# Kernel tuning notes

Measured on AMD Instinct MI355X. Metric: run time of the kernel, lower is better.

Reference implementation:

```python
import jax, jax.numpy as jnp
import numpy as np

N, E, F, D, L, C = 100000, 1600000, 64, 64, 3, 10
BN_EPS = 1e-5


def _batchnorm(h, gamma, beta):
    # training-mode BatchNorm1d: biased batch stats over the node dim
    mu = jnp.mean(h, axis=0)
    var = jnp.mean(jnp.square(h - mu), axis=0)
    return (h - mu) * jax.lax.rsqrt(var + BN_EPS) * gamma + beta


def setup_inputs() -> dict:
    key = jax.random.key(0)
    ks = jax.random.split(key, 6)
    x = jax.random.normal(ks[0], (N, F), jnp.float32)
    edge_index = jax.random.randint(ks[1], (2, E), 0, N, dtype=jnp.int64)
    W1 = jax.random.normal(ks[2], (L, F, D), jnp.float32) * 0.1
    W2 = jax.random.normal(ks[3], (L, D, D), jnp.float32) * 0.1
    fcW = jax.random.normal(ks[4], (L + 1, D, C), jnp.float32) * 0.1
    return {
        "x": x,
        "edge_index": edge_index,
        "W1": W1,
        "b1": jnp.zeros((L, D), jnp.float32),
        "g1": jnp.ones((L, D), jnp.float32),
        "be1": jnp.zeros((L, D), jnp.float32),
        "W2": W2,
        "b2": jnp.zeros((L, D), jnp.float32),
        "gbn": jnp.ones((L, D), jnp.float32),
        "bbn": jnp.zeros((L, D), jnp.float32),
        "fcW": fcW,
        "fcb": jnp.zeros((L + 1, C), jnp.float32),
    }


def reference(x, edge_index, W1, b1, g1, be1, W2, b2, gbn, bbn, fcW, fcb):
    src, dst = edge_index[0], edge_index[1]
    outs = [x]
    h = x
    for i in range(L):
        # GINConv (eps=0): mlp(h + sum_{j in N(i)} h_j)
        agg = jax.ops.segment_sum(h[src], dst, num_segments=N)
        z = (h + agg) @ W1[i] + b1[i]
        z = jax.nn.relu(_batchnorm(z, g1[i], be1[i]))
        z = z @ W2[i] + b2[i]
        # outer BN + ReLU
        h = jax.nn.relu(_batchnorm(z, gbn[i], bbn[i]))
        outs.append(h)
    # jumping-knowledge sum of per-layer classifier heads
    logits = outs[0] @ fcW[0] + fcb[0]
    for i in range(1, L + 1):
        logits = logits + outs[i] @ fcW[i] + fcb[i]
    return jax.nn.log_softmax(logits, axis=-1)
```

## Files before the change

### kernel.cpp

```cpp
#include <hip/hip_runtime.h>
#include <math.h>


#define BN_EPS 1e-5f
#define NBKT 256
#define BCAP 12288
#define PCHUNK 4096

typedef __attribute__((ext_vector_type(8))) short bf16x8;
typedef __attribute__((ext_vector_type(4))) float f32x4;

__device__ __forceinline__ float bf2f(unsigned short u) {
  return __uint_as_float(((unsigned int)u) << 16);
}
__device__ __forceinline__ unsigned short f2bf(float x) {
  unsigned int b = __float_as_uint(x);
  return (unsigned short)((b + 0x7FFFu + ((b >> 16) & 1u)) >> 16);
}

__device__ __forceinline__ float stat8(const float* __restrict__ st, int i) {
  float s = 0.f;
#pragma unroll
  for (int k = 0; k < 8; k++) s += st[k * 128 + i];
  return s;
}


__global__ __launch_bounds__(256) void k_prep(
    const float* __restrict__ W1, const float* __restrict__ W2,
    const float* __restrict__ fcW, unsigned short* __restrict__ wh,
    unsigned short* __restrict__ wl, unsigned short* __restrict__ bh,
    unsigned short* __restrict__ bl) {
  int g = blockIdx.x * 256 + threadIdx.x;
  if (g < 6 * 4096) {
    int m = g >> 12, rem = g & 4095;
    int k = rem >> 6, n = rem & 63;
    const float* W = (m & 1) ? (W2 + (m >> 1) * 4096) : (W1 + (m >> 1) * 4096);
    float w = W[k * 64 + n];
    unsigned short hi = f2bf(w);
    float resid = w - bf2f(hi);
    int kx = (((k >> 3) ^ (n & 7)) << 3) + (k & 7);
    wh[m * 4096 + n * 64 + kx] = hi;
    wl[m * 4096 + n * 64 + kx] = f2bf(resid);
  } else {
    int g2 = g - 6 * 4096;
    if (g2 < 4 * 1024) {
      int l = g2 >> 10, rem = g2 & 1023;
      int n = rem & 15, k = rem >> 4;
      float w = (n < 10) ? fcW[l * 640 + k * 10 + n] : 0.f;
      unsigned short hi = f2bf(w);
      float resid = w - bf2f(hi);
      int idx = l * 1024 + n * 64 + (((k >> 3) ^ (n & 7)) << 3) + (k & 7);
      bh[idx] = hi;
      bl[idx] = f2bf(resid);
    }
  }
}


__global__ __launch_bounds__(256) void k_part_conv(
    const int* __restrict__ src, const int* __restrict__ dst,
    int* __restrict__ bcur, int2* __restrict__ ep, int E, int nparts,
    const float* __restrict__ x, unsigned short* __restrict__ x16, int N) {
  __shared__ int lh[NBKT];
  __shared__ int lbase[NBKT];
  __shared__ int lcur[NBKT];
  int tid = threadIdx.x;
  if ((int)blockIdx.x < nparts) {
    int base = blockIdx.x * PCHUNK;
    int end = min(base + PCHUNK, E);
    lh[tid] = 0;
    lcur[tid] = 0;
    __syncthreads();
    for (int e = base + tid; e < end; e += 256) atomicAdd(&lh[dst[e] >> 9], 1);
    __syncthreads();
    int c = lh[tid];
    lbase[tid] = c ? (tid * BCAP + atomicAdd(&bcur[tid], c)) : 0;
    __syncthreads();
    for (int e = base + tid; e < end; e += 256) {
      int d = dst[e];
      int b = d >> 9;
      int r = atomicAdd(&lcur[b], 1);
      ep[lbase[b] + r] = make_int2(src[e], d);
    }
  } else {
    size_t g = ((size_t)blockIdx.x - nparts) * 256 + tid;
    size_t base = g * 8;
    if (base + 8 <= (size_t)N * 64) {
      float4 t0 = *(const float4*)(x + base);
      float4 t1 = *(const float4*)(x + base + 4);
      *(ushort4*)(x16 + base) =
          make_ushort4(f2bf(t0.x), f2bf(t0.y), f2bf(t0.z), f2bf(t0.w));
      *(ushort4*)(x16 + base + 4) =
          make_ushort4(f2bf(t1.x), f2bf(t1.y), f2bf(t1.z), f2bf(t1.w));
    }
  }
}

__global__ __launch_bounds__(256) void k_bucketsort(
    const int2* __restrict__ ep, const int* __restrict__ bcur,
    int* __restrict__ offs, int* __restrict__ bend, int* __restrict__ csr,
    float* __restrict__ stats) {
  __shared__ int cnt[512];
  __shared__ int ts[256];
  __shared__ int cur[512];
  int t = threadIdx.x;
  int b = blockIdx.x;
  if (b == 0) {
    for (int i = t; i < 6144; i += 256) stats[i] = 0.f;
  }
  int lo = b * BCAP;
  int hi = lo + bcur[b];
  cnt[t] = 0;
  cnt[t + 256] = 0;
  __syncthreads();
  for (int e = lo + t; e < hi; e += 256) atomicAdd(&cnt[ep[e].y & 511], 1);
  __syncthreads();
  int c0 = cnt[2 * t], c1 = cnt[2 * t + 1];
  int s = c0 + c1;
  ts[t] = s;
  __syncthreads();
  for (int o = 1; o < 256; o <<= 1) {
    int add = (t >= o) ? ts[t - o] : 0;
    __syncthreads();
    ts[t] += add;
    __syncthreads();
  }
  int excl = ts[t] - s;
  cur[2 * t] = excl;
  cur[2 * t + 1] = excl + c0;
  int n0 = b << 9;
  offs[n0 + 2 * t] = lo + excl;
  offs[n0 + 2 * t + 1] = lo + excl + c0;
  if (t == 255) bend[b] = lo + ts[255];
  __syncthreads();
  for (int e = lo + t; e < hi; e += 256) {
    int2 p = ep[e];
    int pos = atomicAdd(&cur[p.y & 511], 1);
    csr[lo + pos] = p.x;
  }
}


__device__ __forceinline__ float gather_plain(
    const unsigned short* __restrict__ h16, const int* __restrict__ csr,
    int e0, int e1, int lane) {
  float acc = 0.f;
  int e = e0;
  for (; e + 16 <= e1; e += 16) {
    int s0 = csr[e], s1 = csr[e + 1], s2 = csr[e + 2], s3 = csr[e + 3];
    int s4 = csr[e + 4], s5 = csr[e + 5], s6 = csr[e + 6], s7 = csr[e + 7];
    int s8 = csr[e + 8], s9 = csr[e + 9], sa = csr[e + 10], sb = csr[e + 11];
    int sc = csr[e + 12], sd = csr[e + 13], se = csr[e + 14], sf = csr[e + 15];
    float a0 = bf2f(h16[(size_t)s0 * 64 + lane]);
    float a1 = bf2f(h16[(size_t)s1 * 64 + lane]);
    float a2 = bf2f(h16[(size_t)s2 * 64 + lane]);
    float a3 = bf2f(h16[(size_t)s3 * 64 + lane]);
    float a4 = bf2f(h16[(size_t)s4 * 64 + lane]);
    float a5 = bf2f(h16[(size_t)s5 * 64 + lane]);
    float a6 = bf2f(h16[(size_t)s6 * 64 + lane]);
    float a7 = bf2f(h16[(size_t)s7 * 64 + lane]);
    float a8 = bf2f(h16[(size_t)s8 * 64 + lane]);
    float a9 = bf2f(h16[(size_t)s9 * 64 + lane]);
    float aa = bf2f(h16[(size_t)sa * 64 + lane]);
    float ab = bf2f(h16[(size_t)sb * 64 + lane]);
    float ac = bf2f(h16[(size_t)sc * 64 + lane]);
    float ad = bf2f(h16[(size_t)sd * 64 + lane]);
    float ae = bf2f(h16[(size_t)se * 64 + lane]);
    float af = bf2f(h16[(size_t)sf * 64 + lane]);
    acc += (((a0 + a1) + (a2 + a3)) + ((a4 + a5) + (a6 + a7))) +
           (((a8 + a9) + (aa + ab)) + ((ac + ad) + (ae + af)));
  }
  for (; e + 4 <= e1; e += 4) {
    int s0 = csr[e], s1 = csr[e + 1], s2 = csr[e + 2], s3 = csr[e + 3];
    float a0 = bf2f(h16[(size_t)s0 * 64 + lane]);
    float a1 = bf2f(h16[(size_t)s1 * 64 + lane]);
    float a2 = bf2f(h16[(size_t)s2 * 64 + lane]);
    float a3 = bf2f(h16[(size_t)s3 * 64 + lane]);
    acc += (a0 + a1) + (a2 + a3);
  }
  for (; e < e1; e++) acc += bf2f(h16[(size_t)csr[e] * 64 + lane]);
  return acc;
}

__global__ __launch_bounds__(256) void k_agg(
    const unsigned short* __restrict__ h16, const int* __restrict__ offs,
    const int* __restrict__ bend, const int* __restrict__ csr,
    unsigned short* __restrict__ vout, int N) {
  int gid = blockIdx.x * blockDim.x + threadIdx.x;
  int wid = __builtin_amdgcn_readfirstlane(gid >> 6);
  int lane = threadIdx.x & 63;
  if (wid >= N) return;
  int e0 = offs[wid];
  int e1 = ((wid & 511) == 511) ? bend[wid >> 9] : offs[wid + 1];
  float acc = bf2f(h16[(size_t)wid * 64 + lane]) +
              gather_plain(h16, csr, e0, e1, lane);
  vout[(size_t)wid * 64 + lane] = f2bf(acc);
}

__global__ __launch_bounds__(256) void k_aggbn(
    const unsigned short* __restrict__ z16,
    const float* __restrict__ stats_in, const float* __restrict__ gv,
    const float* __restrict__ bev,
    const int* __restrict__ offs, const int* __restrict__ bend,
    const int* __restrict__ csr, unsigned short* __restrict__ vout, int N) {
  __shared__ float ABs[128];
  int tid = threadIdx.x;
  if (tid < 64) {
    float inv_n = 1.f / (float)N;
    float mu = stat8(stats_in, tid) * inv_n;
    float var = stat8(stats_in, 64 + tid) * inv_n - mu * mu;
    float A = rsqrtf(var + BN_EPS) * gv[tid];
    ABs[tid] = A;
    ABs[64 + tid] = bev[tid] - mu * A;
  }
  __syncthreads();
  int gid = blockIdx.x * blockDim.x + tid;
  int wid = __builtin_amdgcn_readfirstlane(gid >> 6);
  int lane = tid & 63;
  if (wid >= N) return;
  float A = ABs[lane], B = ABs[64 + lane];
  float acc = fmaxf(bf2f(z16[(size_t)wid * 64 + lane]) * A + B, 0.f);
  int e0 = offs[wid];
  int e1 = ((wid & 511) == 511) ? bend[wid >> 9] : offs[wid + 1];
  int e = e0;
  for (; e + 16 <= e1; e += 16) {
    int s0 = csr[e], s1 = csr[e + 1], s2 = csr[e + 2], s3 = csr[e + 3];
    int s4 = csr[e + 4], s5 = csr[e + 5], s6 = csr[e + 6], s7 = csr[e + 7];
    int s8 = csr[e + 8], s9 = csr[e + 9], sa = csr[e + 10], sb = csr[e + 11];
    int sc = csr[e + 12], sd = csr[e + 13], se = csr[e + 14], sf = csr[e + 15];
    float a0 = bf2f(z16[(size_t)s0 * 64 + lane]);
    float a1 = bf2f(z16[(size_t)s1 * 64 + lane]);
    float a2 = bf2f(z16[(size_t)s2 * 64 + lane]);
    float a3 = bf2f(z16[(size_t)s3 * 64 + lane]);
    float a4 = bf2f(z16[(size_t)s4 * 64 + lane]);
    float a5 = bf2f(z16[(size_t)s5 * 64 + lane]);
    float a6 = bf2f(z16[(size_t)s6 * 64 + lane]);
    float a7 = bf2f(z16[(size_t)s7 * 64 + lane]);
    float a8 = bf2f(z16[(size_t)s8 * 64 + lane]);
    float a9 = bf2f(z16[(size_t)s9 * 64 + lane]);
    float aa = bf2f(z16[(size_t)sa * 64 + lane]);
    float ab = bf2f(z16[(size_t)sb * 64 + lane]);
    float ac = bf2f(z16[(size_t)sc * 64 + lane]);
    float ad = bf2f(z16[(size_t)sd * 64 + lane]);
    float ae = bf2f(z16[(size_t)se * 64 + lane]);
    float af = bf2f(z16[(size_t)sf * 64 + lane]);
    a0 = fmaxf(a0 * A + B, 0.f); a1 = fmaxf(a1 * A + B, 0.f);
    a2 = fmaxf(a2 * A + B, 0.f); a3 = fmaxf(a3 * A + B, 0.f);
    a4 = fmaxf(a4 * A + B, 0.f); a5 = fmaxf(a5 * A + B, 0.f);
    a6 = fmaxf(a6 * A + B, 0.f); a7 = fmaxf(a7 * A + B, 0.f);
    a8 = fmaxf(a8 * A + B, 0.f); a9 = fmaxf(a9 * A + B, 0.f);
    aa = fmaxf(aa * A + B, 0.f); ab = fmaxf(ab * A + B, 0.f);
    ac = fmaxf(ac * A + B, 0.f); ad = fmaxf(ad * A + B, 0.f);
    ae = fmaxf(ae * A + B, 0.f); af = fmaxf(af * A + B, 0.f);
    acc += (((a0 + a1) + (a2 + a3)) + ((a4 + a5) + (a6 + a7))) +
           (((a8 + a9) + (aa + ab)) + ((ac + ad) + (ae + af)));
  }
  for (; e + 4 <= e1; e += 4) {
    int s0 = csr[e], s1 = csr[e + 1], s2 = csr[e + 2], s3 = csr[e + 3];
    float a0 = bf2f(z16[(size_t)s0 * 64 + lane]);
    float a1 = bf2f(z16[(size_t)s1 * 64 + lane]);
    float a2 = bf2f(z16[(size_t)s2 * 64 + lane]);
    float a3 = bf2f(z16[(size_t)s3 * 64 + lane]);
    a0 = fmaxf(a0 * A + B, 0.f); a1 = fmaxf(a1 * A + B, 0.f);
    a2 = fmaxf(a2 * A + B, 0.f); a3 = fmaxf(a3 * A + B, 0.f);
    acc += (a0 + a1) + (a2 + a3);
  }
  for (; e < e1; e++) {
    float a = bf2f(z16[(size_t)csr[e] * 64 + lane]);
    acc += fmaxf(a * A + B, 0.f);
  }
  vout[(size_t)wid * 64 + lane] = f2bf(acc);
}

__global__ __launch_bounds__(256) void k_gemm2(
    const unsigned short* __restrict__ vin, unsigned short* __restrict__ zout,
    const unsigned short* __restrict__ Wh, const unsigned short* __restrict__ Wl,
    const float* __restrict__ stats_in, const float* __restrict__ gv,
    const float* __restrict__ bev, int dobn,
    float* __restrict__ stats_out, int N) {
  __shared__ float ABs[128];
  __shared__ float red[512];
  int tid = threadIdx.x;
  int n0 = blockIdx.x * 256;
  if (dobn) {
    if (tid < 64) {
      float inv_n = 1.f / (float)N;
      float mu = stat8(stats_in, tid) * inv_n;
      float var = stat8(stats_in, 64 + tid) * inv_n - mu * mu;
      float A = rsqrtf(var + BN_EPS) * gv[tid];
      ABs[tid] = A;
      ABs[64 + tid] = bev[tid] - mu * A;
    }
    __syncthreads();
  }

  int wv = tid >> 6;
  int lane = tid & 63;
  int c = lane & 15;
  int q = lane >> 4;
  int wrow = n0 + wv * 64;

  bf16x8 afrag[4][2];
#pragma unroll
  for (int mt = 0; mt < 4; mt++) {
    int row = wrow + mt * 16 + c;
#pragma unroll
    for (int kb = 0; kb < 2; kb++) {
      int col0 = kb * 32 + q * 8;
      bf16x8 a = {0, 0, 0, 0, 0, 0, 0, 0};
      if (row < N) {
        a = *(const bf16x8*)(vin + (size_t)row * 64 + col0);
        if (dobn) {
#pragma unroll
          for (int j = 0; j < 8; j++) {
            float f = bf2f((unsigned short)a[j]) * ABs[col0 + j] +
                      ABs[64 + col0 + j];
            a[j] = (short)f2bf(fmaxf(f, 0.f));
          }
        }
      }
      afrag[mt][kb] = a;
    }
  }

  f32x4 acc[4][4];
#pragma unroll
  for (int mt = 0; mt < 4; mt++)
#pragma unroll
    for (int nt = 0; nt < 4; nt++)
      acc[mt][nt] = (f32x4){0.f, 0.f, 0.f, 0.f};

#pragma unroll
  for (int nt = 0; nt < 4; nt++) {
    int cn = nt * 16 + c;
#pragma unroll
    for (int kb = 0; kb < 2; kb++) {
      int kchunk = kb * 4 + q;
      int kx = ((kchunk ^ (cn & 7)) << 3);
      bf16x8 bhi = *(const bf16x8*)(Wh + cn * 64 + kx);
      bf16x8 blo = *(const bf16x8*)(Wl + cn * 64 + kx);
#pragma unroll
      for (int mt = 0; mt < 4; mt++) {
        acc[mt][nt] = __builtin_amdgcn_mfma_f32_16x16x32_bf16(
            afrag[mt][kb], bhi, acc[mt][nt], 0, 0, 0);
        acc[mt][nt] = __builtin_amdgcn_mfma_f32_16x16x32_bf16(
            afrag[mt][kb], blo, acc[mt][nt], 0, 0, 0);
      }
    }
  }

#pragma unroll
  for (int mt = 0; mt < 4; mt++) {
#pragma unroll
    for (int r = 0; r < 4; r++) {
      int row = wrow + mt * 16 + q * 4 + r;
      if (row < N) {
        unsigned short* zr = zout + (size_t)row * 64 + c;
        zr[0] = f2bf(acc[mt][0][r]);
        zr[16] = f2bf(acc[mt][1][r]);
        zr[32] = f2bf(acc[mt][2][r]);
        zr[48] = f2bf(acc[mt][3][r]);
      }
    }
  }

  float cs[4], cq[4];
#pragma unroll
  for (int nt = 0; nt < 4; nt++) {
    float s = 0.f, s2 = 0.f;
#pragma unroll
    for (int mt = 0; mt < 4; mt++)
#pragma unroll
      for (int r = 0; r < 4; r++) {
        float v = acc[mt][nt][r];
        s += v;
        s2 += v * v;
      }
    s += __shfl_xor(s, 16);
    s += __shfl_xor(s, 32);
    s2 += __shfl_xor(s2, 16);
    s2 += __shfl_xor(s2, 32);
    cs[nt] = s;
    cq[nt] = s2;
  }
  if (lane < 16) {
#pragma unroll
    for (int nt = 0; nt < 4; nt++) {
      red[wv * 128 + nt * 16 + lane] = cs[nt];
      red[wv * 128 + 64 + nt * 16 + lane] = cq[nt];
    }
  }
  __syncthreads();
  if (tid < 64) {
    float a = red[tid] + red[128 + tid] + red[256 + tid] + red[384 + tid];
    float b = red[64 + tid] + red[192 + tid] + red[320 + tid] + red[448 + tid];
    float* so = stats_out + (blockIdx.x & 7) * 128;
    atomicAdd(&so[tid], a);
    atomicAdd(&so[64 + tid], b);
  }
}

__global__ __launch_bounds__(256) void k_head_mfma(
    const unsigned short* __restrict__ x16,
    const unsigned short* __restrict__ z0, const unsigned short* __restrict__ z1,
    const unsigned short* __restrict__ z2, const float* __restrict__ stats,
    const float* __restrict__ gbn, const float* __restrict__ bbn,
    const unsigned short* __restrict__ bh, const unsigned short* __restrict__ bl,
    const float* __restrict__ fcb, float* __restrict__ out, int N) {
  __shared__ float ABs[3 * 128];
  int tid = threadIdx.x;
  if (tid < 64) {
    float inv_n = 1.f / (float)N;
#pragma unroll
    for (int l = 0; l < 3; l++) {
      const float* st = stats + (2 * l + 1) * 1024;
      float mu = stat8(st, tid) * inv_n;
      float var = stat8(st, 64 + tid) * inv_n - mu * mu;
      float A = rsqrtf(var + BN_EPS) * gbn[l * 64 + tid];
      ABs[l * 128 + tid] = A;
      ABs[l * 128 + 64 + tid] = bbn[l * 64 + tid] - mu * A;
    }
  }
  __syncthreads();

  int wv = tid >> 6, lane = tid & 63;
  int c = lane & 15, q = lane >> 4;
  int wrow = blockIdx.x * 128 + wv * 32;

  f32x4 acc[2];
  acc[0] = (f32x4){0.f, 0.f, 0.f, 0.f};
  acc[1] = (f32x4){0.f, 0.f, 0.f, 0.f};
#pragma unroll
  for (int l = 0; l < 4; l++) {
    const unsigned short* z = (l == 0) ? x16 : (l == 1) ? z0 : (l == 2) ? z1
                                                                       : z2;
#pragma unroll
    for (int kb = 0; kb < 2; kb++) {
      int kchunk = kb * 4 + q;
      int kx = ((kchunk ^ (c & 7)) << 3);
      bf16x8 bh_ = *(const bf16x8*)(bh + l * 1024 + c * 64 + kx);
      bf16x8 bl_ = *(const bf16x8*)(bl + l * 1024 + c * 64 + kx);
      int col0 = kb * 32 + q * 8;
#pragma unroll
      for (int mt = 0; mt < 2; mt++) {
        int row = wrow + mt * 16 + c;
        bf16x8 a = {0, 0, 0, 0, 0, 0, 0, 0};
        if (row < N) {
          a = *(const bf16x8*)(z + (size_t)row * 64 + col0);
          if (l > 0) {
            const float* AB = ABs + (l - 1) * 128;
#pragma unroll
            for (int j = 0; j < 8; j++) {
              float f = bf2f((unsigned short)a[j]) * AB[col0 + j] +
                        AB[64 + col0 + j];
              a[j] = (short)f2bf(fmaxf(f, 0.f));
            }
          }
        }
        acc[mt] = __builtin_amdgcn_mfma_f32_16x16x32_bf16(a, bh_, acc[mt],
                                                          0, 0, 0);
        acc[mt] = __builtin_amdgcn_mfma_f32_16x16x32_bf16(a, bl_, acc[mt],
                                                          0, 0, 0);
      }
    }
  }
  float cb = 0.f;
  if (c < 10) cb = fcb[c] + fcb[10 + c] + fcb[20 + c] + fcb[30 + c];
#pragma unroll
  for (int mt = 0; mt < 2; mt++) {
    float v[4], vm[4];
#pragma unroll
    for (int r = 0; r < 4; r++) {
      v[r] = acc[mt][r] + cb;
      vm[r] = (c < 10) ? v[r] : -INFINITY;
    }
#pragma unroll
    for (int off = 1; off < 16; off <<= 1) {
#pragma unroll
      for (int r = 0; r < 4; r++) vm[r] = fmaxf(vm[r], __shfl_xor(vm[r], off));
    }
    float sm[4];
#pragma unroll
    for (int r = 0; r < 4; r++) sm[r] = (c < 10) ? expf(v[r] - vm[r]) : 0.f;
#pragma unroll
    for (int off = 1; off < 16; off <<= 1) {
#pragma unroll
      for (int r = 0; r < 4; r++) sm[r] += __shfl_xor(sm[r], off);
    }
#pragma unroll
    for (int r = 0; r < 4; r++) {
      int row = wrow + mt * 16 + q * 4 + r;
      if (row < N && c < 10)
        out[(size_t)row * 10 + c] = v[r] - (logf(sm[r]) + vm[r]);
    }
  }
}

extern "C" void kernel_launch(void* const* d_in, const int* in_sizes, int n_in,
                              void* d_out, int out_size, void* d_ws, size_t ws_size,
                              hipStream_t stream) {
  const float* x = (const float*)d_in[0];
  const int* ei = (const int*)d_in[1];
  const float* W1 = (const float*)d_in[2];
  const float* g1 = (const float*)d_in[4];
  const float* be1 = (const float*)d_in[5];
  const float* W2 = (const float*)d_in[6];
  const float* gbn = (const float*)d_in[8];
  const float* bbn = (const float*)d_in[9];
  const float* fcW = (const float*)d_in[10];
  const float* fcb = (const float*)d_in[11];
  float* out = (float*)d_out;

  const int N = in_sizes[0] / 64;
  const int E = in_sizes[1] / 2;
  const int* src = ei;
  const int* dst = ei + E;

  char* ws = (char*)d_ws;
  size_t off = 0;
  auto alloc = [&](size_t bytes) -> void* {
    void* p = ws + off;
    off = (off + bytes + 255) & ~(size_t)255;
    return p;
  };
  int* bcur = (int*)alloc(NBKT * 4);
  float* stats = (float*)alloc(6 * 1024 * 4);
  int* offs = (int*)alloc((size_t)NBKT * 512 * 4);
  int* bend = (int*)alloc(NBKT * 4);
  int* csr = (int*)alloc((size_t)NBKT * BCAP * 4);
  unsigned short* w16h = (unsigned short*)alloc(6 * 4096 * 2);
  unsigned short* w16l = (unsigned short*)alloc(6 * 4096 * 2);
  unsigned short* bh16 = (unsigned short*)alloc(4 * 1024 * 2);
  unsigned short* bl16 = (unsigned short*)alloc(4 * 1024 * 2);
  unsigned short* x16 = (unsigned short*)alloc((size_t)N * 64 * 2);
  unsigned short* v16 = (unsigned short*)alloc((size_t)N * 64 * 2);
  unsigned short* z1_16 = (unsigned short*)alloc((size_t)N * 64 * 2);
  unsigned short* z16a = (unsigned short*)alloc((size_t)N * 64 * 2);
  unsigned short* z16b = (unsigned short*)alloc((size_t)N * 64 * 2);
  unsigned short* z16c = (unsigned short*)alloc((size_t)N * 64 * 2);
  int2* ep = (int2*)alloc((size_t)NBKT * BCAP * 8);
  (void)ws_size;
  (void)n_in;
  (void)out_size;

  unsigned short* z16l_[3] = {z16a, z16b, z16c};
  int gb = (N + 127) / 128;
  int gb2 = (N + 255) / 256;
  int ab = (N * 64 + 255) / 256;
  int nparts = (E + PCHUNK - 1) / PCHUNK;
  int nconv = (N * 64 / 8 + 255) / 256;
  hipMemsetAsync(bcur, 0, NBKT * 4, stream);
  k_prep<<<112, 256, 0, stream>>>(W1, W2, fcW, w16h, w16l, bh16, bl16);
  k_part_conv<<<nparts + nconv, 256, 0, stream>>>(src, dst, bcur, ep, E,
                                                  nparts, x, x16, N);
  k_bucketsort<<<NBKT, 256, 0, stream>>>(ep, bcur, offs, bend, csr, stats);

  for (int l = 0; l < 3; l++) {
    float* st1 = stats + (2 * l) * 1024;
    float* st2 = stats + (2 * l + 1) * 1024;
    if (l == 0) {
      k_agg<<<ab, 256, 0, stream>>>(x16, offs, bend, csr, v16, N);
    } else {
      float* st2p = stats + (2 * (l - 1) + 1) * 1024;
      k_aggbn<<<ab, 256, 0, stream>>>(z16l_[l - 1], st2p, gbn + (l - 1) * 64,
                                      bbn + (l - 1) * 64, offs, bend, csr,
                                      v16, N);
    }
    k_gemm2<<<gb2, 256, 0, stream>>>(v16, z1_16, w16h + (2 * l) * 4096,
                                     w16l + (2 * l) * 4096, nullptr, nullptr,
                                     nullptr, 0, st1, N);
    k_gemm2<<<gb2, 256, 0, stream>>>(z1_16, z16l_[l], w16h + (2 * l + 1) * 4096,
                                     w16l + (2 * l + 1) * 4096, st1,
                                     g1 + l * 64, be1 + l * 64, 1, st2, N);
  }
  k_head_mfma<<<gb, 256, 0, stream>>>(x16, z16a, z16b, z16c, stats, gbn, bbn,
                                      bh16, bl16, fcb, out, N);
}
```

Before: 349.8 us.

## Fuse neighbor aggregation with first GEMM and widen BN stat slots

The per-layer aggregation kernel and the first MLP GEMM are merged into one kernel. Each wave gathers 16 nodes into LDS, then runs bf16 MFMA (hi/lo split weights) and accumulates the BatchNorm statistics. This drops the v16 intermediate round trip through global memory and one launch per layer. Stats atomics are spread over 32 slots instead of 8 to ease contention, since the grid now has more blocks, at the cost of longer stat reductions. The gather now runs as a sequential per-wave loop over 16 nodes, which may reduce memory-level parallelism.

```diff
diff --git a/kernel.cpp b/kernel.cpp
--- a/kernel.cpp
+++ b/kernel.cpp
@@ -6,6 +6,7 @@
 #define NBKT 256
 #define BCAP 12288
 #define PCHUNK 4096
+#define NSLOT 32
 
 typedef __attribute__((ext_vector_type(8))) short bf16x8;
 typedef __attribute__((ext_vector_type(4))) float f32x4;
@@ -18,10 +19,10 @@
   return (unsigned short)((b + 0x7FFFu + ((b >> 16) & 1u)) >> 16);
 }
 
-__device__ __forceinline__ float stat8(const float* __restrict__ st, int i) {
+__device__ __forceinline__ float stat32(const float* __restrict__ st, int i) {
   float s = 0.f;
 #pragma unroll
-  for (int k = 0; k < 8; k++) s += st[k * 128 + i];
+  for (int k = 0; k < NSLOT; k++) s += st[k * 128 + i];
   return s;
 }
 
@@ -107,7 +108,7 @@
   int t = threadIdx.x;
   int b = blockIdx.x;
   if (b == 0) {
-    for (int i = t; i < 6144; i += 256) stats[i] = 0.f;
+    for (int i = t; i < 6 * NSLOT * 128; i += 256) stats[i] = 0.f;
   }
   int lo = b * BCAP;
   int hi = lo + bcur[b];
@@ -183,68 +184,32 @@
   return acc;
 }
 
-__global__ __launch_bounds__(256) void k_agg(
-    const unsigned short* __restrict__ h16, const int* __restrict__ offs,
-    const int* __restrict__ bend, const int* __restrict__ csr,
-    unsigned short* __restrict__ vout, int N) {
-  int gid = blockIdx.x * blockDim.x + threadIdx.x;
-  int wid = __builtin_amdgcn_readfirstlane(gid >> 6);
-  int lane = threadIdx.x & 63;
-  if (wid >= N) return;
-  int e0 = offs[wid];
-  int e1 = ((wid & 511) == 511) ? bend[wid >> 9] : offs[wid + 1];
-  float acc = bf2f(h16[(size_t)wid * 64 + lane]) +
-              gather_plain(h16, csr, e0, e1, lane);
-  vout[(size_t)wid * 64 + lane] = f2bf(acc);
-}
-
-__global__ __launch_bounds__(256) void k_aggbn(
-    const unsigned short* __restrict__ z16,
-    const float* __restrict__ stats_in, const float* __restrict__ gv,
-    const float* __restrict__ bev,
-    const int* __restrict__ offs, const int* __restrict__ bend,
-    const int* __restrict__ csr, unsigned short* __restrict__ vout, int N) {
-  __shared__ float ABs[128];
-  int tid = threadIdx.x;
-  if (tid < 64) {
-    float inv_n = 1.f / (float)N;
-    float mu = stat8(stats_in, tid) * inv_n;
-    float var = stat8(stats_in, 64 + tid) * inv_n - mu * mu;
-    float A = rsqrtf(var + BN_EPS) * gv[tid];
-    ABs[tid] = A;
-    ABs[64 + tid] = bev[tid] - mu * A;
-  }
-  __syncthreads();
-  int gid = blockIdx.x * blockDim.x + tid;
-  int wid = __builtin_amdgcn_readfirstlane(gid >> 6);
-  int lane = tid & 63;
-  if (wid >= N) return;
-  float A = ABs[lane], B = ABs[64 + lane];
-  float acc = fmaxf(bf2f(z16[(size_t)wid * 64 + lane]) * A + B, 0.f);
-  int e0 = offs[wid];
-  int e1 = ((wid & 511) == 511) ? bend[wid >> 9] : offs[wid + 1];
+__device__ __forceinline__ float gather_bn(
+    const unsigned short* __restrict__ h16, const int* __restrict__ csr,
+    int e0, int e1, int lane, float A, float B) {
+  float acc = 0.f;
   int e = e0;
   for (; e + 16 <= e1; e += 16) {
     int s0 = csr[e], s1 = csr[e + 1], s2 = csr[e + 2], s3 = csr[e + 3];
     int s4 = csr[e + 4], s5 = csr[e + 5], s6 = csr[e + 6], s7 = csr[e + 7];
     int s8 = csr[e + 8], s9 = csr[e + 9], sa = csr[e + 10], sb = csr[e + 11];
     int sc = csr[e + 12], sd = csr[e + 13], se = csr[e + 14], sf = csr[e + 15];
-    float a0 = bf2f(z16[(size_t)s0 * 64 + lane]);
-    float a1 = bf2f(z16[(size_t)s1 * 64 + lane]);
-    float a2 = bf2f(z16[(size_t)s2 * 64 + lane]);
-    float a3 = bf2f(z16[(size_t)s3 * 64 + lane]);
-    float a4 = bf2f(z16[(size_t)s4 * 64 + lane]);
-    float a5 = bf2f(z16[(size_t)s5 * 64 + lane]);
-    float a6 = bf2f(z16[(size_t)s6 * 64 + lane]);
-    float a7 = bf2f(z16[(size_t)s7 * 64 + lane]);
-    float a8 = bf2f(z16[(size_t)s8 * 64 + lane]);
-    float a9 = bf2f(z16[(size_t)s9 * 64 + lane]);
-    float aa = bf2f(z16[(size_t)sa * 64 + lane]);
-    float ab = bf2f(z16[(size_t)sb * 64 + lane]);
-    float ac = bf2f(z16[(size_t)sc * 64 + lane]);
-    float ad = bf2f(z16[(size_t)sd * 64 + lane]);
-    float ae = bf2f(z16[(size_t)se * 64 + lane]);
-    float af = bf2f(z16[(size_t)sf * 64 + lane]);
+    float a0 = bf2f(h16[(size_t)s0 * 64 + lane]);
+    float a1 = bf2f(h16[(size_t)s1 * 64 + lane]);
+    float a2 = bf2f(h16[(size_t)s2 * 64 + lane]);
+    float a3 = bf2f(h16[(size_t)s3 * 64 + lane]);
+    float a4 = bf2f(h16[(size_t)s4 * 64 + lane]);
+    float a5 = bf2f(h16[(size_t)s5 * 64 + lane]);
+    float a6 = bf2f(h16[(size_t)s6 * 64 + lane]);
+    float a7 = bf2f(h16[(size_t)s7 * 64 + lane]);
+    float a8 = bf2f(h16[(size_t)s8 * 64 + lane]);
+    float a9 = bf2f(h16[(size_t)s9 * 64 + lane]);
+    float aa = bf2f(h16[(size_t)sa * 64 + lane]);
+    float ab = bf2f(h16[(size_t)sb * 64 + lane]);
+    float ac = bf2f(h16[(size_t)sc * 64 + lane]);
+    float ad = bf2f(h16[(size_t)sd * 64 + lane]);
+    float ae = bf2f(h16[(size_t)se * 64 + lane]);
+    float af = bf2f(h16[(size_t)sf * 64 + lane]);
     a0 = fmaxf(a0 * A + B, 0.f); a1 = fmaxf(a1 * A + B, 0.f);
     a2 = fmaxf(a2 * A + B, 0.f); a3 = fmaxf(a3 * A + B, 0.f);
     a4 = fmaxf(a4 * A + B, 0.f); a5 = fmaxf(a5 * A + B, 0.f);
@@ -258,19 +223,133 @@
   }
   for (; e + 4 <= e1; e += 4) {
     int s0 = csr[e], s1 = csr[e + 1], s2 = csr[e + 2], s3 = csr[e + 3];
-    float a0 = bf2f(z16[(size_t)s0 * 64 + lane]);
-    float a1 = bf2f(z16[(size_t)s1 * 64 + lane]);
-    float a2 = bf2f(z16[(size_t)s2 * 64 + lane]);
-    float a3 = bf2f(z16[(size_t)s3 * 64 + lane]);
+    float a0 = bf2f(h16[(size_t)s0 * 64 + lane]);
+    float a1 = bf2f(h16[(size_t)s1 * 64 + lane]);
+    float a2 = bf2f(h16[(size_t)s2 * 64 + lane]);
+    float a3 = bf2f(h16[(size_t)s3 * 64 + lane]);
     a0 = fmaxf(a0 * A + B, 0.f); a1 = fmaxf(a1 * A + B, 0.f);
     a2 = fmaxf(a2 * A + B, 0.f); a3 = fmaxf(a3 * A + B, 0.f);
     acc += (a0 + a1) + (a2 + a3);
   }
   for (; e < e1; e++) {
-    float a = bf2f(z16[(size_t)csr[e] * 64 + lane]);
+    float a = bf2f(h16[(size_t)csr[e] * 64 + lane]);
     acc += fmaxf(a * A + B, 0.f);
   }
-  vout[(size_t)wid * 64 + lane] = f2bf(acc);
+  return acc;
+}
+
+template <bool DOBN>
+__global__ __launch_bounds__(256) void k_aggemm(
+    const unsigned short* __restrict__ h16, const float* __restrict__ stats_in,
+    const float* __restrict__ gv, const float* __restrict__ bev,
+    const int* __restrict__ offs, const int* __restrict__ bend,
+    const int* __restrict__ csr, const unsigned short* __restrict__ Wh,
+    const unsigned short* __restrict__ Wl, unsigned short* __restrict__ zout,
+    float* __restrict__ stats_out, int N) {
+  __shared__ float ABs[128];
+  __shared__ float red[512];
+  __shared__ __align__(16) unsigned short vlds[64 * 72];
+  int tid = threadIdx.x;
+  if (DOBN) {
+    if (tid < 64) {
+      float inv_n = 1.f / (float)N;
+      float mu = stat32(stats_in, tid) * inv_n;
+      float var = stat32(stats_in, 64 + tid) * inv_n - mu * mu;
+      float A = rsqrtf(var + BN_EPS) * gv[tid];
+      ABs[tid] = A;
+      ABs[64 + tid] = bev[tid] - mu * A;
+    }
+    __syncthreads();
+  }
+  int wv = tid >> 6, lane = tid & 63;
+  int nbase = blockIdx.x * 64 + wv * 16;
+  float A = DOBN ? ABs[lane] : 1.f;
+  float B = DOBN ? ABs[64 + lane] : 0.f;
+  unsigned short* vw = vlds + (size_t)wv * 16 * 72;
+
+#pragma unroll 1
+  for (int i = 0; i < 16; i++) {
+    int node = nbase + i;
+    float val = 0.f;
+    if (node < N) {
+      int e0 = offs[node];
+      int e1 = ((node & 511) == 511) ? bend[node >> 9] : offs[node + 1];
+      float sv = bf2f(h16[(size_t)node * 64 + lane]);
+      if (DOBN) {
+        val = fmaxf(sv * A + B, 0.f) + gather_bn(h16, csr, e0, e1, lane, A, B);
+      } else {
+        val = sv + gather_plain(h16, csr, e0, e1, lane);
+      }
+    }
+    vw[i * 72 + lane] = f2bf(val);
+  }
+
+  int c = lane & 15, q = lane >> 4;
+  bf16x8 af[2];
+#pragma unroll
+  for (int kb = 0; kb < 2; kb++)
+    af[kb] = *(const bf16x8*)(vlds + ((size_t)wv * 16 + c) * 72 + kb * 32 +
+                              q * 8);
+  f32x4 acc[4];
+#pragma unroll
+  for (int nt = 0; nt < 4; nt++) acc[nt] = (f32x4){0.f, 0.f, 0.f, 0.f};
+#pragma unroll
+  for (int nt = 0; nt < 4; nt++) {
+    int cn = nt * 16 + c;
+#pragma unroll
+    for (int kb = 0; kb < 2; kb++) {
+      int kx = (((kb * 4 + q) ^ (cn & 7)) << 3);
+      bf16x8 bhi = *(const bf16x8*)(Wh + cn * 64 + kx);
+      bf16x8 blo = *(const bf16x8*)(Wl + cn * 64 + kx);
+      acc[nt] = __builtin_amdgcn_mfma_f32_16x16x32_bf16(af[kb], bhi, acc[nt],
+                                                        0, 0, 0);
+      acc[nt] = __builtin_amdgcn_mfma_f32_16x16x32_bf16(af[kb], blo, acc[nt],
+                                                        0, 0, 0);
+    }
+  }
+#pragma unroll
+  for (int r = 0; r < 4; r++) {
+    int row = nbase + q * 4 + r;
+    if (row < N) {
+      unsigned short* zr = zout + (size_t)row * 64 + c;
+      zr[0] = f2bf(acc[0][r]);
+      zr[16] = f2bf(acc[1][r]);
+      zr[32] = f2bf(acc[2][r]);
+      zr[48] = f2bf(acc[3][r]);
+    }
+  }
+  float cs[4], cq[4];
+#pragma unroll
+  for (int nt = 0; nt < 4; nt++) {
+    float s = 0.f, s2 = 0.f;
+#pragma unroll
+    for (int r = 0; r < 4; r++) {
+      float v = acc[nt][r];
+      s += v;
+      s2 += v * v;
+    }
+    s += __shfl_xor(s, 16);
+    s += __shfl_xor(s, 32);
+    s2 += __shfl_xor(s2, 16);
+    s2 += __shfl_xor(s2, 32);
+    cs[nt] = s;
+    cq[nt] = s2;
+  }
+  if (lane < 16) {
+#pragma unroll
+    for (int nt = 0; nt < 4; nt++) {
+      red[wv * 128 + nt * 16 + lane] = cs[nt];
+      red[wv * 128 + 64 + nt * 16 + lane] = cq[nt];
+    }
+  }
+  __syncthreads();
+  if (tid < 64) {
+    float a = red[tid] + red[128 + tid] + red[256 + tid] + red[384 + tid];
+    float b = red[64 + tid] + red[192 + tid] + red[320 + tid] + red[448 + tid];
+    float* so = stats_out + (blockIdx.x & (NSLOT - 1)) * 128;
+    atomicAdd(&so[tid], a);
+    atomicAdd(&so[64 + tid], b);
+  }
 }
 
 __global__ __launch_bounds__(256) void k_gemm2(
@@ -286,8 +365,8 @@
   if (dobn) {
     if (tid < 64) {
       float inv_n = 1.f / (float)N;
-      float mu = stat8(stats_in, tid) * inv_n;
-      float var = stat8(stats_in, 64 + tid) * inv_n - mu * mu;
+      float mu = stat32(stats_in, tid) * inv_n;
+      float var = stat32(stats_in, 64 + tid) * inv_n - mu * mu;
       float A = rsqrtf(var + BN_EPS) * gv[tid];
       ABs[tid] = A;
       ABs[64 + tid] = bev[tid] - mu * A;
@@ -395,7 +474,7 @@
   if (tid < 64) {
     float a = red[tid] + red[128 + tid] + red[256 + tid] + red[384 + tid];
     float b = red[64 + tid] + red[192 + tid] + red[320 + tid] + red[448 + tid];
-    float* so = stats_out + (blockIdx.x & 7) * 128;
+    float* so = stats_out + (blockIdx.x & (NSLOT - 1)) * 128;
     atomicAdd(&so[tid], a);
     atomicAdd(&so[64 + tid], b);
   }
@@ -414,9 +493,9 @@
     float inv_n = 1.f / (float)N;
 #pragma unroll
     for (int l = 0; l < 3; l++) {
-      const float* st = stats + (2 * l + 1) * 1024;
-      float mu = stat8(st, tid) * inv_n;
-      float var = stat8(st, 64 + tid) * inv_n - mu * mu;
+      const float* st = stats + (2 * l + 1) * (NSLOT * 128);
+      float mu = stat32(st, tid) * inv_n;
+      float var = stat32(st, 64 + tid) * inv_n - mu * mu;
       float A = rsqrtf(var + BN_EPS) * gbn[l * 64 + tid];
       ABs[l * 128 + tid] = A;
       ABs[l * 128 + 64 + tid] = bbn[l * 64 + tid] - mu * A;
@@ -525,7 +604,7 @@
     return p;
   };
   int* bcur = (int*)alloc(NBKT * 4);
-  float* stats = (float*)alloc(6 * 1024 * 4);
+  float* stats = (float*)alloc(6 * NSLOT * 128 * 4);
   int* offs = (int*)alloc((size_t)NBKT * 512 * 4);
   int* bend = (int*)alloc(NBKT * 4);
   int* csr = (int*)alloc((size_t)NBKT * BCAP * 4);
@@ -534,7 +613,6 @@
   unsigned short* bh16 = (unsigned short*)alloc(4 * 1024 * 2);
   unsigned short* bl16 = (unsigned short*)alloc(4 * 1024 * 2);
   unsigned short* x16 = (unsigned short*)alloc((size_t)N * 64 * 2);
-  unsigned short* v16 = (unsigned short*)alloc((size_t)N * 64 * 2);
   unsigned short* z1_16 = (unsigned short*)alloc((size_t)N * 64 * 2);
   unsigned short* z16a = (unsigned short*)alloc((size_t)N * 64 * 2);
   unsigned short* z16b = (unsigned short*)alloc((size_t)N * 64 * 2);
@@ -547,7 +625,7 @@
   unsigned short* z16l_[3] = {z16a, z16b, z16c};
   int gb = (N + 127) / 128;
   int gb2 = (N + 255) / 256;
-  int ab = (N * 64 + 255) / 256;
+  int fb = (N + 63) / 64;
   int nparts = (E + PCHUNK - 1) / PCHUNK;
   int nconv = (N * 64 / 8 + 255) / 256;
   hipMemsetAsync(bcur, 0, NBKT * 4, stream);
@@ -557,19 +635,19 @@
   k_bucketsort<<<NBKT, 256, 0, stream>>>(ep, bcur, offs, bend, csr, stats);
 
   for (int l = 0; l < 3; l++) {
-    float* st1 = stats + (2 * l) * 1024;
-    float* st2 = stats + (2 * l + 1) * 1024;
+    float* st1 = stats + (2 * l) * (NSLOT * 128);
+    float* st2 = stats + (2 * l + 1) * (NSLOT * 128);
     if (l == 0) {
-      k_agg<<<ab, 256, 0, stream>>>(x16, offs, bend, csr, v16, N);
+      k_aggemm<false><<<fb, 256, 0, stream>>>(
+          x16, nullptr, nullptr, nullptr, offs, bend, csr,
+          w16h + (2 * l) * 4096, w16l + (2 * l) * 4096, z1_16, st1, N);
     } else {
-      float* st2p = stats + (2 * (l - 1) + 1) * 1024;
-      k_aggbn<<<ab, 256, 0, stream>>>(z16l_[l - 1], st2p, gbn + (l - 1) * 64,
-                                      bbn + (l - 1) * 64, offs, bend, csr,
-                                      v16, N);
-    }
-    k_gemm2<<<gb2, 256, 0, stream>>>(v16, z1_16, w16h + (2 * l) * 4096,
-                                     w16l + (2 * l) * 4096, nullptr, nullptr,
-                                     nullptr, 0, st1, N);
+      float* st2p = stats + (2 * (l - 1) + 1) * (NSLOT * 128);
+      k_aggemm<true><<<fb, 256, 0, stream>>>(
+          z16l_[l - 1], st2p, gbn + (l - 1) * 64, bbn + (l - 1) * 64, offs,
+          bend, csr, w16h + (2 * l) * 4096, w16l + (2 * l) * 4096, z1_16, st1,
+          N);
+    }
     k_gemm2<<<gb2, 256, 0, stream>>>(z1_16, z16l_[l], w16h + (2 * l + 1) * 4096,
                                      w16l + (2 * l + 1) * 4096, st1,
                                      g1 + l * 64, be1 + l * 64, 1, st2, N);
```

Result: slower. 479.4 us (+37.1%).
